# Kernel optimization log

Measured on AMD Instinct MI355X. Metric: run time of the kernel, lower is better.

## Reference

```python
import jax, jax.numpy as jnp
import numpy as np


def hat_so3(v):
    # v: [..., 3] -> skew-symmetric [..., 3, 3]
    vx, vy, vz = v[..., 0], v[..., 1], v[..., 2]
    z = jnp.zeros_like(vx)
    r0 = jnp.stack([z, -vz, vy], axis=-1)
    r1 = jnp.stack([vz, z, -vx], axis=-1)
    r2 = jnp.stack([-vy, vx, z], axis=-1)
    return jnp.stack([r0, r1, r2], axis=-2)


def vee_so3(m):
    # m: [..., 3, 3] skew -> [..., 3]
    return jnp.stack([m[..., 2, 1], m[..., 0, 2], m[..., 1, 0]], axis=-1)


def setup_inputs() -> dict:
    key = jax.random.key(0)
    k1, k2, k3, k4, k5 = jax.random.split(key, 5)
    B, F, K, N = 8, 256, 3, 4096
    x = jax.random.normal(k1, (B, F, K, N), dtype=jnp.float32)
    M1 = jax.random.normal(k2, (3, 3), dtype=jnp.float32)
    M2 = jax.random.normal(k3, (3, 3), dtype=jnp.float32)
    W1 = jax.random.normal(k4, (F, F), dtype=jnp.float32) * (1.0 / np.sqrt(F))
    W2 = jax.random.normal(k5, (F, F), dtype=jnp.float32) * (1.0 / np.sqrt(F))
    return {"x": x, "M1": M1, "M2": M2, "W1": W1, "W2": W2}


def reference(x, M1, M2, W1, W2):
    # learn_dir: Linear over channel dim F (no bias): y[b,g,k,n] = sum_f x[b,f,k,n] * W[g,f]
    d = jnp.einsum('bfkn,gf->bgkn', x, W1)
    d2 = jnp.einsum('bfkn,gf->bgkn', x, W2)
    # rotate by M1/M2 and move K=3 to last dim: [B,F,N,3]
    d = jnp.einsum('dk,bfkn->bfnd', M1, d)
    d2 = jnp.einsum('dk,bfkn->bfnd', M2, d2)
    d_hat = hat_so3(d)        # [B,F,N,3,3]
    d2_hat = hat_so3(d2)      # [B,F,N,3,3]
    lie_bracket = jnp.matmul(d2_hat, d_hat) - jnp.matmul(d_hat, d2_hat)
    v = vee_so3(lie_bracket)  # [B,F,N,3]
    return x + jnp.swapaxes(v, 2, 3)  # [B,F,3,N]
```

## Files before the change

kernel.cpp:

```cpp
#include <hip/hip_runtime.h>
#include <hip/hip_bf16.h>

#define B_  8
#define F_  256
#define N_  4096
#define BN  32
#define THREADS 512

typedef __attribute__((ext_vector_type(8))) short short8;
typedef __attribute__((ext_vector_type(4))) float f32x4;
typedef __attribute__((ext_vector_type(4))) unsigned short us4;

__device__ inline unsigned short f2bf(float f) {
    union { float f; unsigned int u; } c; c.f = f;
    unsigned int u = c.u;
    unsigned int r = u + 0x7FFFu + ((u >> 16) & 1u);
    return (unsigned short)(r >> 16);
}
__device__ inline unsigned int pack2(float a, float b) {
    return (unsigned int)f2bf(a) | ((unsigned int)f2bf(b) << 16);
}
__device__ inline float bf2f(unsigned short h) {
    union { unsigned int u; float f; } c; c.u = ((unsigned int)h) << 16;
    return c.f;
}

__global__ void wconv_kernel(const float* __restrict__ W1,
                             const float* __restrict__ W2,
                             unsigned short* __restrict__ Wb) {
    int t = blockIdx.x * blockDim.x + threadIdx.x;
    int e = t * 8;
    const float* src = (e & 65536) ? W2 : W1;
    int rem = e & 65535;
    float4 a = *(const float4*)(src + rem);
    float4 b = *(const float4*)(src + rem + 4);
    short8 o;
    o[0] = (short)f2bf(a.x); o[1] = (short)f2bf(a.y);
    o[2] = (short)f2bf(a.z); o[3] = (short)f2bf(a.w);
    o[4] = (short)f2bf(b.x); o[5] = (short)f2bf(b.y);
    o[6] = (short)f2bf(b.z); o[7] = (short)f2bf(b.w);
    *(short8*)(Wb + e) = o;
}

__global__ __launch_bounds__(THREADS, 4) void lie_fused_kernel(
    const float* __restrict__ x, const float* __restrict__ M1,
    const float* __restrict__ M2, const unsigned short* __restrict__ Wb,
    float* __restrict__ out)
{
    __shared__ unsigned short Xs[48 * 68 * 8];

    const int tid  = threadIdx.x;
    const int wave = tid >> 6;
    const int lane = tid & 63;
    const int c16  = lane & 15;
    const int quad = lane >> 4;

    const int bid   = blockIdx.x;
    const int gh    = bid & 1;
    const int ntile = (bid >> 1) & 127;
    const int b     = bid >> 8;
    const int n0    = ntile * BN;

    const float* xb = x + (size_t)b * F_ * 3 * N_ + n0;

    #pragma unroll
    for (int i = 0; i < 6; i++) {
        int pc  = tid + THREADS * i;
        int q   = pc & 7;
        int fpl = (pc >> 3) & 7;
        int rr  = pc >> 6;
        int k   = rr % 3;
        int fph = rr / 3;
        int f0  = (fph * 8 + fpl) * 2;
        const float* p0 = xb + (size_t)(f0 * 3 + k) * N_ + q * 4;
        float4 va = *(const float4*)p0;
        float4 vb = *(const float4*)(p0 + 3 * N_);
        int ch = f0 >> 5;
        int ct = k * 2 + (q >> 2);
        int qp = (f0 & 31) >> 3;
        int U0 = (ch * 6 + ct) * 68 + (q & 3) * 4 + 16 * qp + qp;
        unsigned int* dst = (unsigned int*)((char*)Xs + U0 * 16 + (f0 & 7) * 2);
        dst[0]  = pack2(va.x, vb.x);
        dst[4]  = pack2(va.y, vb.y);
        dst[8]  = pack2(va.z, vb.z);
        dst[12] = pack2(va.w, vb.w);
    }

    f32x4 acc[2][6];
    #pragma unroll
    for (int wi = 0; wi < 2; wi++)
        #pragma unroll
        for (int ct = 0; ct < 6; ct++)
            acc[wi][ct] = (f32x4)(0.f);

    const int gRow = gh * 128 + wave * 16 + c16;
    const unsigned short* wb0 = Wb + gRow * 256 + quad * 8;

    __syncthreads();

    short8 Ac0 = *(const short8*)(wb0);
    short8 Ac1 = *(const short8*)(wb0 + 65536);
    #pragma unroll
    for (int ch = 0; ch < 8; ch++) {
        short8 An0, An1;
        if (ch < 7) {
            An0 = *(const short8*)(wb0 + (ch + 1) * 32);
            An1 = *(const short8*)(wb0 + 65536 + (ch + 1) * 32);
        }
        short8 bf[6];
        #pragma unroll
        for (int ct = 0; ct < 6; ct++)
            bf[ct] = *(const short8*)((char*)Xs
                        + (size_t)((ch * 6 + ct) * 68 + lane + quad) * 16);
        #pragma unroll
        for (int ct = 0; ct < 6; ct++)
            acc[0][ct] = __builtin_amdgcn_mfma_f32_16x16x32_bf16(Ac0, bf[ct], acc[0][ct], 0, 0, 0);
        #pragma unroll
        for (int ct = 0; ct < 6; ct++)
            acc[1][ct] = __builtin_amdgcn_mfma_f32_16x16x32_bf16(Ac1, bf[ct], acc[1][ct], 0, 0, 0);
        if (ch < 7) { Ac0 = An0; Ac1 = An1; }
    }

    float m1v[9], m2v[9];
    #pragma unroll
    for (int i = 0; i < 9; i++) { m1v[i] = M1[i]; m2v[i] = M2[i]; }

    const int gq  = gh * 128 + wave * 16 + quad * 4;
    const int j0  = (quad & 1) * 4;
    const int qpp = (gq & 31) >> 3;
    const int chg = gq >> 5;

    #pragma unroll
    for (int ct0 = 0; ct0 < 2; ct0++) {
        const int n = n0 + ct0 * 16 + c16;
        us4 rx[3];
        #pragma unroll
        for (int k = 0; k < 3; k++) {
            int U = (chg * 6 + k * 2 + ct0) * 68 + c16 + 16 * qpp + qpp;
            rx[k] = *(const us4*)((char*)Xs + (size_t)U * 16 + j0 * 2);
        }
        #pragma unroll
        for (int r = 0; r < 4; r++) {
            const int g = gq + r;
            float c1x = acc[0][ct0 + 0][r];
            float c1y = acc[0][ct0 + 2][r];
            float c1z = acc[0][ct0 + 4][r];
            float c2x = acc[1][ct0 + 0][r];
            float c2y = acc[1][ct0 + 2][r];
            float c2z = acc[1][ct0 + 4][r];
            float d0 = m1v[0]*c1x + m1v[1]*c1y + m1v[2]*c1z;
            float d1 = m1v[3]*c1x + m1v[4]*c1y + m1v[5]*c1z;
            float d2 = m1v[6]*c1x + m1v[7]*c1y + m1v[8]*c1z;
            float e0 = m2v[0]*c2x + m2v[1]*c2y + m2v[2]*c2z;
            float e1 = m2v[3]*c2x + m2v[4]*c2y + m2v[5]*c2z;
            float e2 = m2v[6]*c2x + m2v[7]*c2y + m2v[8]*c2z;
            float v0 = e1 * d2 - e2 * d1;
            float v1 = e2 * d0 - e0 * d2;
            float v2 = e0 * d1 - e1 * d0;
            const size_t base = ((size_t)(b * F_ + g) * 3) * N_ + n;
            out[base + 0 * (size_t)N_] = bf2f(rx[0][r]) + v0;
            out[base + 1 * (size_t)N_] = bf2f(rx[1][r]) + v1;
            out[base + 2 * (size_t)N_] = bf2f(rx[2][r]) + v2;
        }
    }
}

extern "C" void kernel_launch(void* const* d_in, const int* in_sizes, int n_in,
                              void* d_out, int out_size, void* d_ws, size_t ws_size,
                              hipStream_t stream) {
    const float* x  = (const float*)d_in[0];
    const float* M1 = (const float*)d_in[1];
    const float* M2 = (const float*)d_in[2];
    const float* W1 = (const float*)d_in[3];
    const float* W2 = (const float*)d_in[4];
    float* out = (float*)d_out;
    unsigned short* Wb = (unsigned short*)d_ws;

    wconv_kernel<<<64, 256, 0, stream>>>(W1, W2, Wb);
    lie_fused_kernel<<<2048, THREADS, 0, stream>>>(x, M1, M2, Wb, out);
}
```

Before: 221.2 us.

## Make fused kernel persistent with double-buffered x tiles and full-F output per block

Replaces the 2048-block grid with a 256-block persistent grid in which each block processes 8 tiles of 16 columns covering all 256 output channels. The next tile's x loads are issued into registers before the current tile's MFMA work, and a double-buffered LDS tile lets writing and computing alternate. This removes the earlier split of output channels across two blocks, which loaded each x tile twice, and aims to hide global load latency. In exchange the column tile is narrower, more accumulators and prefetch registers are live, occupancy drops to 2 blocks per CU, and there is a single barrier per tile.

After: 212.6 us. 3.9% less time.

```diff
diff --git a/kernel.cpp b/kernel.cpp
--- a/kernel.cpp
+++ b/kernel.cpp
@@ -4,8 +4,12 @@
 #define B_  8
 #define F_  256
 #define N_  4096
-#define BN  32
+#define BN  16
+#define TPB 8
+#define GRID 256
 #define THREADS 512
+#define TSTRIDE 1088
+#define BUFU (24 * 68)
 
 typedef __attribute__((ext_vector_type(8))) short short8;
 typedef __attribute__((ext_vector_type(4))) float f32x4;
@@ -42,12 +46,37 @@
     *(short8*)(Wb + e) = o;
 }
 
-__global__ __launch_bounds__(THREADS, 4) void lie_fused_kernel(
+__device__ inline void load_tile(const float* __restrict__ xb, int fp, int q,
+                                 float4* ra, float4* rb) {
+    #pragma unroll
+    for (int it = 0; it < 3; it++) {
+        const float* p = xb + (size_t)(6 * fp + it) * N_ + q * 4;
+        ra[it] = *(const float4*)p;
+        rb[it] = *(const float4*)(p + 3 * N_);
+    }
+}
+
+__device__ inline void write_tile(char* __restrict__ buf, int ch_s, int qw,
+                                  int dd, int q, const float4* ra, const float4* rb) {
+    #pragma unroll
+    for (int it = 0; it < 3; it++) {
+        char* tbase = buf + (ch_s * 3 + it) * TSTRIDE + dd * 4;
+        const float* fa = (const float*)&ra[it];
+        const float* fb = (const float*)&rb[it];
+        #pragma unroll
+        for (int dn = 0; dn < 4; dn++) {
+            int uu = qw * 16 + q * 4 + dn;
+            *(unsigned int*)(tbase + (uu + qw) * 16) = pack2(fa[dn], fb[dn]);
+        }
+    }
+}
+
+__global__ __launch_bounds__(THREADS, 2) void lie_fused_kernel(
     const float* __restrict__ x, const float* __restrict__ M1,
     const float* __restrict__ M2, const unsigned short* __restrict__ Wb,
     float* __restrict__ out)
 {
-    __shared__ unsigned short Xs[48 * 68 * 8];
+    __shared__ uint4 Xs[2][BUFU];
 
     const int tid  = threadIdx.x;
     const int wave = tid >> 6;
@@ -55,113 +84,115 @@
     const int c16  = lane & 15;
     const int quad = lane >> 4;
 
-    const int bid   = blockIdx.x;
-    const int gh    = bid & 1;
-    const int ntile = (bid >> 1) & 127;
-    const int b     = bid >> 8;
-    const int n0    = ntile * BN;
-
-    const float* xb = x + (size_t)b * F_ * 3 * N_ + n0;
-
-    #pragma unroll
-    for (int i = 0; i < 6; i++) {
-        int pc  = tid + THREADS * i;
-        int q   = pc & 7;
-        int fpl = (pc >> 3) & 7;
-        int rr  = pc >> 6;
-        int k   = rr % 3;
-        int fph = rr / 3;
-        int f0  = (fph * 8 + fpl) * 2;
-        const float* p0 = xb + (size_t)(f0 * 3 + k) * N_ + q * 4;
-        float4 va = *(const float4*)p0;
-        float4 vb = *(const float4*)(p0 + 3 * N_);
-        int ch = f0 >> 5;
-        int ct = k * 2 + (q >> 2);
-        int qp = (f0 & 31) >> 3;
-        int U0 = (ch * 6 + ct) * 68 + (q & 3) * 4 + 16 * qp + qp;
-        unsigned int* dst = (unsigned int*)((char*)Xs + U0 * 16 + (f0 & 7) * 2);
-        dst[0]  = pack2(va.x, vb.x);
-        dst[4]  = pack2(va.y, vb.y);
-        dst[8]  = pack2(va.z, vb.z);
-        dst[12] = pack2(va.w, vb.w);
-    }
-
-    f32x4 acc[2][6];
-    #pragma unroll
-    for (int wi = 0; wi < 2; wi++)
-        #pragma unroll
-        for (int ct = 0; ct < 6; ct++)
-            acc[wi][ct] = (f32x4)(0.f);
-
-    const int gRow = gh * 128 + wave * 16 + c16;
-    const unsigned short* wb0 = Wb + gRow * 256 + quad * 8;
-
-    __syncthreads();
-
-    short8 Ac0 = *(const short8*)(wb0);
-    short8 Ac1 = *(const short8*)(wb0 + 65536);
-    #pragma unroll
-    for (int ch = 0; ch < 8; ch++) {
-        short8 An0, An1;
-        if (ch < 7) {
-            An0 = *(const short8*)(wb0 + (ch + 1) * 32);
-            An1 = *(const short8*)(wb0 + 65536 + (ch + 1) * 32);
-        }
-        short8 bf[6];
-        #pragma unroll
-        for (int ct = 0; ct < 6; ct++)
-            bf[ct] = *(const short8*)((char*)Xs
-                        + (size_t)((ch * 6 + ct) * 68 + lane + quad) * 16);
-        #pragma unroll
-        for (int ct = 0; ct < 6; ct++)
-            acc[0][ct] = __builtin_amdgcn_mfma_f32_16x16x32_bf16(Ac0, bf[ct], acc[0][ct], 0, 0, 0);
-        #pragma unroll
-        for (int ct = 0; ct < 6; ct++)
-            acc[1][ct] = __builtin_amdgcn_mfma_f32_16x16x32_bf16(Ac1, bf[ct], acc[1][ct], 0, 0, 0);
-        if (ch < 7) { Ac0 = An0; Ac1 = An1; }
-    }
+    const int fp   = tid >> 2;
+    const int q    = tid & 3;
+    const int ch_s = fp >> 4;
+    const int fpl  = fp & 15;
+    const int qw   = fpl >> 2;
+    const int dd   = fpl & 3;
+
+    const int rdoff = (lane + (lane >> 4)) * 16;
+
+    const unsigned short* wbase = Wb + (wave * 32 + c16) * 256 + quad * 8;
 
     float m1v[9], m2v[9];
     #pragma unroll
     for (int i = 0; i < 9; i++) { m1v[i] = M1[i]; m2v[i] = M2[i]; }
 
-    const int gq  = gh * 128 + wave * 16 + quad * 4;
-    const int j0  = (quad & 1) * 4;
-    const int qpp = (gq & 31) >> 3;
-    const int chg = gq >> 5;
-
-    #pragma unroll
-    for (int ct0 = 0; ct0 < 2; ct0++) {
-        const int n = n0 + ct0 * 16 + c16;
-        us4 rx[3];
-        #pragma unroll
-        for (int k = 0; k < 3; k++) {
-            int U = (chg * 6 + k * 2 + ct0) * 68 + c16 + 16 * qpp + qpp;
-            rx[k] = *(const us4*)((char*)Xs + (size_t)U * 16 + j0 * 2);
-        }
-        #pragma unroll
-        for (int r = 0; r < 4; r++) {
-            const int g = gq + r;
-            float c1x = acc[0][ct0 + 0][r];
-            float c1y = acc[0][ct0 + 2][r];
-            float c1z = acc[0][ct0 + 4][r];
-            float c2x = acc[1][ct0 + 0][r];
-            float c2y = acc[1][ct0 + 2][r];
-            float c2z = acc[1][ct0 + 4][r];
-            float d0 = m1v[0]*c1x + m1v[1]*c1y + m1v[2]*c1z;
-            float d1 = m1v[3]*c1x + m1v[4]*c1y + m1v[5]*c1z;
-            float d2 = m1v[6]*c1x + m1v[7]*c1y + m1v[8]*c1z;
-            float e0 = m2v[0]*c2x + m2v[1]*c2y + m2v[2]*c2z;
-            float e1 = m2v[3]*c2x + m2v[4]*c2y + m2v[5]*c2z;
-            float e2 = m2v[6]*c2x + m2v[7]*c2y + m2v[8]*c2z;
-            float v0 = e1 * d2 - e2 * d1;
-            float v1 = e2 * d0 - e0 * d2;
-            float v2 = e0 * d1 - e1 * d0;
-            const size_t base = ((size_t)(b * F_ + g) * 3) * N_ + n;
-            out[base + 0 * (size_t)N_] = bf2f(rx[0][r]) + v0;
-            out[base + 1 * (size_t)N_] = bf2f(rx[1][r]) + v1;
-            out[base + 2 * (size_t)N_] = bf2f(rx[2][r]) + v2;
-        }
+    float4 ra[3], rb[3];
+
+    int task = blockIdx.x;
+    {
+        const float* xb = x + (size_t)(task >> 8) * 768 * N_ + (task & 255) * BN;
+        load_tile(xb, fp, q, ra, rb);
+    }
+
+    for (int t = 0; t < TPB; t++) {
+        char* buf = (char*)Xs[t & 1];
+
+        write_tile(buf, ch_s, qw, dd, q, ra, rb);
+        __syncthreads();
+
+        const int b  = task >> 8;
+        const int nt = task & 255;
+        const int next = task + GRID;
+
+        if (t < TPB - 1) {
+            const float* xb = x + (size_t)(next >> 8) * 768 * N_ + (next & 255) * BN;
+            load_tile(xb, fp, q, ra, rb);
+        }
+
+        f32x4 acc[2][2][3];
+        #pragma unroll
+        for (int wi = 0; wi < 2; wi++)
+            #pragma unroll
+            for (int gt = 0; gt < 2; gt++)
+                #pragma unroll
+                for (int k = 0; k < 3; k++)
+                    acc[wi][gt][k] = (f32x4)(0.f);
+
+        short8 a00 = *(const short8*)(wbase);
+        short8 a01 = *(const short8*)(wbase + 4096);
+        short8 a10 = *(const short8*)(wbase + 65536);
+        short8 a11 = *(const short8*)(wbase + 69632);
+        #pragma unroll
+        for (int ch = 0; ch < 8; ch++) {
+            short8 n00, n01, n10, n11;
+            if (ch < 7) {
+                n00 = *(const short8*)(wbase + (ch + 1) * 32);
+                n01 = *(const short8*)(wbase + 4096 + (ch + 1) * 32);
+                n10 = *(const short8*)(wbase + 65536 + (ch + 1) * 32);
+                n11 = *(const short8*)(wbase + 69632 + (ch + 1) * 32);
+            }
+            short8 bfr[3];
+            #pragma unroll
+            for (int k = 0; k < 3; k++)
+                bfr[k] = *(const short8*)(buf + (ch * 3 + k) * TSTRIDE + rdoff);
+            #pragma unroll
+            for (int k = 0; k < 3; k++) {
+                acc[0][0][k] = __builtin_amdgcn_mfma_f32_16x16x32_bf16(a00, bfr[k], acc[0][0][k], 0, 0, 0);
+                acc[0][1][k] = __builtin_amdgcn_mfma_f32_16x16x32_bf16(a01, bfr[k], acc[0][1][k], 0, 0, 0);
+                acc[1][0][k] = __builtin_amdgcn_mfma_f32_16x16x32_bf16(a10, bfr[k], acc[1][0][k], 0, 0, 0);
+                acc[1][1][k] = __builtin_amdgcn_mfma_f32_16x16x32_bf16(a11, bfr[k], acc[1][1][k], 0, 0, 0);
+            }
+            if (ch < 7) { a00 = n00; a01 = n01; a10 = n10; a11 = n11; }
+        }
+
+        float* ob = out + (size_t)b * 768 * N_ + nt * BN + c16;
+        #pragma unroll
+        for (int gt = 0; gt < 2; gt++) {
+            us4 rx[3];
+            const int qp = gt * 2 + (quad >> 1);
+            #pragma unroll
+            for (int k = 0; k < 3; k++) {
+                int uu = qp * 16 + c16;
+                rx[k] = *(const us4*)(buf + (wave * 3 + k) * TSTRIDE
+                           + (uu + qp) * 16 + (quad & 1) * 8);
+            }
+            #pragma unroll
+            for (int r = 0; r < 4; r++) {
+                const int g = wave * 32 + gt * 16 + quad * 4 + r;
+                float c1x = acc[0][gt][0][r];
+                float c1y = acc[0][gt][1][r];
+                float c1z = acc[0][gt][2][r];
+                float c2x = acc[1][gt][0][r];
+                float c2y = acc[1][gt][1][r];
+                float c2z = acc[1][gt][2][r];
+                float d0 = m1v[0]*c1x + m1v[1]*c1y + m1v[2]*c1z;
+                float d1 = m1v[3]*c1x + m1v[4]*c1y + m1v[5]*c1z;
+                float d2 = m1v[6]*c1x + m1v[7]*c1y + m1v[8]*c1z;
+                float e0 = m2v[0]*c2x + m2v[1]*c2y + m2v[2]*c2z;
+                float e1 = m2v[3]*c2x + m2v[4]*c2y + m2v[5]*c2z;
+                float e2 = m2v[6]*c2x + m2v[7]*c2y + m2v[8]*c2z;
+                float v0 = e1 * d2 - e2 * d1;
+                float v1 = e2 * d0 - e0 * d2;
+                float v2 = e0 * d1 - e1 * d0;
+                ob[(size_t)(g * 3 + 0) * N_] = bf2f(rx[0][r]) + v0;
+                ob[(size_t)(g * 3 + 1) * N_] = bf2f(rx[1][r]) + v1;
+                ob[(size_t)(g * 3 + 2) * N_] = bf2f(rx[2][r]) + v2;
+            }
+        }
+        task = next;
     }
 }
 
@@ -177,5 +208,5 @@
     unsigned short* Wb = (unsigned short*)d_ws;
 
     wconv_kernel<<<64, 256, 0, stream>>>(W1, W2, Wb);
-    lie_fused_kernel<<<2048, THREADS, 0, stream>>>(x, M1, M2, Wb, out);
-}
+    lie_fused_kernel<<<GRID, THREADS, 0, stream>>>(x, M1, M2, Wb, out);
+}
```
